# Kernel optimization log

Measured on AMD Instinct MI355X. Metric: run time of the kernel, lower is better.

Reference implementation:

```python
import jax, jax.numpy as jnp
import numpy as np

N_NODES = 100000
N_EDGES = 600000
D = 128  # input_dim == output_dim (required by index_add into zeros_like(x) + residual)
EPS = 1e-5


def _linear_params(key, d_in, d_out):
    kw, kb = jax.random.split(key)
    bound = 1.0 / np.sqrt(d_in)
    w = jax.random.uniform(kw, (d_in, d_out), minval=-bound, maxval=bound, dtype=jnp.float32)
    b = jax.random.uniform(kb, (d_out,), minval=-bound, maxval=bound, dtype=jnp.float32)
    return w, b


def setup_inputs() -> dict:
    key = jax.random.key(0)
    ks = jax.random.split(key, 6)
    x = jax.random.normal(ks[0], (N_NODES, D), dtype=jnp.float32)
    edge_index = jax.random.randint(ks[1], (2, N_EDGES), 0, N_NODES, dtype=jnp.int32)
    w_m1, b_m1 = _linear_params(ks[2], 2 * D, D)
    w_m2, b_m2 = _linear_params(ks[3], D, D)
    w_u1, b_u1 = _linear_params(ks[4], 2 * D, D)
    w_u2, b_u2 = _linear_params(ks[5], D, D)
    gamma = jnp.ones((D,), dtype=jnp.float32)
    beta = jnp.zeros((D,), dtype=jnp.float32)
    return {
        "x": x, "edge_index": edge_index,
        "w_m1": w_m1, "b_m1": b_m1, "w_m2": w_m2, "b_m2": b_m2,
        "w_u1": w_u1, "b_u1": b_u1, "w_u2": w_u2, "b_u2": b_u2,
        "gamma": gamma, "beta": beta,
    }


def _layernorm(h, gamma, beta):
    mu = jnp.mean(h, axis=-1, keepdims=True)
    var = jnp.mean(jnp.square(h - mu), axis=-1, keepdims=True)
    return (h - mu) * jax.lax.rsqrt(var + EPS) * gamma + beta


def reference(x, edge_index, w_m1, b_m1, w_m2, b_m2, w_u1, b_u1, w_u2, b_u2, gamma, beta):
    row, col = edge_index[0], edge_index[1]
    # message MLP on concat of gathered endpoints: [E, 2D] -> [E, D]
    m_in = jnp.concatenate([x[row], x[col]], axis=-1)
    m = jax.nn.relu(m_in @ w_m1 + b_m1) @ w_m2 + b_m2
    # scatter-add messages to destination nodes (index_add along dim 0 with col)
    agg = jax.ops.segment_sum(m, col, num_segments=x.shape[0])
    # update MLP on [N, 2D] -> [N, D]
    u_in = jnp.concatenate([x, agg], axis=-1)
    h = jax.nn.relu(u_in @ w_u1 + b_u1) @ w_u2 + b_u2
    return _layernorm(h, gamma, beta) + x
```

## Files before the change

kernel.cpp:

```cpp
#include <hip/hip_runtime.h>
#include <hip/hip_bf16.h>
#include <stdint.h>

#define N_NODES 100000
#define N_EDGES 600000
#define D 128
#define EPS 1e-5f
#define SCAN_BS 512
#define ROW_MASK 0x1FFFF

#define PREP_BLOCKS 321
#define HIST_BLOCKS 2344
#define XF_BLOCKS   3125
#define SC_BLOCKS   2344
#define AU_BLOCKS   3125

typedef __attribute__((ext_vector_type(8))) short short8;
typedef __attribute__((ext_vector_type(16))) float floatx16;


__device__ __forceinline__ uint32_t pack_bf16_rne(float lo, float hi) {
    uint32_t ul = __builtin_bit_cast(uint32_t, lo);
    uint32_t uh = __builtin_bit_cast(uint32_t, hi);
    ul += 0x7fffu + ((ul >> 16) & 1u);
    uh += 0x7fffu + ((uh >> 16) & 1u);
    return (ul >> 16) | (uh & 0xffff0000u);
}

__device__ __forceinline__ unsigned short f32_to_bf16_rne(float f) {
    uint32_t u = __builtin_bit_cast(uint32_t, f);
    u += 0x7fffu + ((u >> 16) & 1u);
    return (unsigned short)(u >> 16);
}

__device__ __forceinline__ float bflo(uint32_t a) { return __builtin_bit_cast(float, a << 16); }
__device__ __forceinline__ float bfhi(uint32_t a) { return __builtin_bit_cast(float, a & 0xffff0000u); }

__global__ void prep_hist(const float* __restrict__ w_m1, const float* __restrict__ w_u1,
                          const float* __restrict__ w_u2, const float* __restrict__ w_m2,
                          const float* __restrict__ b_m2,
                          unsigned short* __restrict__ wm1f, unsigned short* __restrict__ wu1tf,
                          unsigned short* __restrict__ wu2f, unsigned short* __restrict__ wcf,
                          float* __restrict__ vb,
                          const int* __restrict__ col, int* __restrict__ count,
                          int* __restrict__ rank) {
    if (blockIdx.x >= PREP_BLOCKS) {
        int e = (blockIdx.x - PREP_BLOCKS) * 256 + threadIdx.x;
        if (e < N_EDGES) rank[e] = atomicAdd(&count[col[e]], 1);
        return;
    }
    int idx = blockIdx.x * 256 + threadIdx.x;
    if (idx < 32768) {
        int j = idx & 7, lane = (idx >> 3) & 63, t = (idx >> 9) & 3, s = idx >> 11;
        int kk = s * 16 + ((lane >> 5) << 3) + j;
        wm1f[idx] = f32_to_bf16_rne(w_m1[kk * 128 + t * 32 + (lane & 31)]);
    } else if (idx < 49152) {
        int ii = idx - 32768;
        int j = ii & 7, lane = (ii >> 3) & 63, t = (ii >> 9) & 3, s = ii >> 11;
        int kk = s * 16 + ((lane >> 5) << 3) + j;
        wu1tf[ii] = f32_to_bf16_rne(w_u1[kk * 128 + t * 32 + (lane & 31)]);
    } else if (idx < 65536) {
        int ii = idx - 49152;
        int j = ii & 7, lane = (ii >> 3) & 63, t = (ii >> 9) & 3, s = ii >> 11;
        int kk = s * 16 + ((lane >> 5) << 3) + j;
        wu2f[ii] = f32_to_bf16_rne(w_u2[kk * 128 + t * 32 + (lane & 31)]);
    } else if (idx < 81920) {
        int ii = idx - 65536;
        int j = ii & 7, lane = (ii >> 3) & 63, t = (ii >> 9) & 3, s = ii >> 11;
        int kk = s * 16 + ((lane >> 5) << 3) + j;
        int nn = t * 32 + (lane & 31);
        float acc = 0.0f;
        for (int q = 0; q < 128; ++q)
            acc += w_m2[kk * 128 + q] * w_u1[(128 + q) * 128 + nn];
        wcf[ii] = f32_to_bf16_rne(acc);
    } else if (idx < 82048) {
        int nn = idx - 81920;
        float acc = 0.0f;
        for (int q = 0; q < 128; ++q)
            acc += b_m2[q] * w_u1[(128 + q) * 128 + nn];
        vb[nn] = acc;
    }
}

__global__ void scan_one(const int* __restrict__ count, int* __restrict__ base,
                         int* __restrict__ gcur) {
    __shared__ int tmp[SCAN_BS];
    __shared__ int bbase;
    int g = blockIdx.x * SCAN_BS + threadIdx.x;
    int v = (g < N_NODES) ? count[g] : 0;
    tmp[threadIdx.x] = v;
    __syncthreads();
    int acc = v;
#pragma unroll
    for (int off = 1; off < SCAN_BS; off <<= 1) {
        int add = (threadIdx.x >= off) ? tmp[threadIdx.x - off] : 0;
        __syncthreads();
        acc += add;
        tmp[threadIdx.x] = acc;
        __syncthreads();
    }
    if (threadIdx.x == SCAN_BS - 1) bbase = atomicAdd(gcur, acc);
    __syncthreads();
    if (g < N_NODES) base[g] = bbase + acc - v;
}

__launch_bounds__(64, 4)
__global__ void xform_scatter(const float* __restrict__ x, const short8* __restrict__ w1f,
                              const float* __restrict__ b1, unsigned short* __restrict__ xtb,
                              const int* __restrict__ row, const int* __restrict__ col,
                              const int* __restrict__ rank, const int* __restrict__ base,
                              int* __restrict__ srow) {
    if (blockIdx.x >= XF_BLOCKS) {
        int e4 = (((blockIdx.x - XF_BLOCKS) * 64 + threadIdx.x) << 2);
        if (e4 < N_EDGES) {
            int4 r4 = *(const int4*)(row + e4);
            int4 c4 = *(const int4*)(col + e4);
            int4 k4 = *(const int4*)(rank + e4);
            srow[base[c4.x] + k4.x] = r4.x | ((c4.x & 31) << 17);
            srow[base[c4.y] + k4.y] = r4.y | ((c4.y & 31) << 17);
            srow[base[c4.z] + k4.z] = r4.z | ((c4.z & 31) << 17);
            srow[base[c4.w] + k4.w] = r4.w | ((c4.w & 31) << 17);
        }
        return;
    }

    __shared__ __align__(16) short h1[32 * 136];
    const int lane = threadIdx.x;
    const int l31  = lane & 31;
    const int half = lane >> 5;
    short* hl = h1;

    const int nbase = blockIdx.x * 32;
    const int n = nbase + l31;
    const float* px = x + (size_t)n * D + half * 8;

    union { short8 v; uint32_t u[4]; } fa[8];
#pragma unroll
    for (int s = 0; s < 8; ++s) {
        const int off = s * 16;
        float4 a0 = *(const float4*)(px + off);
        float4 a1 = *(const float4*)(px + off + 4);
        fa[s].u[0] = pack_bf16_rne(a0.x, a0.y); fa[s].u[1] = pack_bf16_rne(a0.z, a0.w);
        fa[s].u[2] = pack_bf16_rne(a1.x, a1.y); fa[s].u[3] = pack_bf16_rne(a1.z, a1.w);
    }

#pragma unroll
    for (int p = 0; p < 2; ++p) {
        floatx16 acc[4];
#pragma unroll
        for (int t = 0; t < 4; ++t) acc[t] = (floatx16)0.0f;
#pragma unroll
        for (int s = 0; s < 8; ++s) {
#pragma unroll
            for (int t = 0; t < 4; ++t) {
                short8 wf = w1f[((p * 8 + s) * 4 + t) * 64 + lane];
                acc[t] = __builtin_amdgcn_mfma_f32_32x32x16_bf16(fa[s].v, wf, acc[t], 0, 0, 0);
            }
        }
#pragma unroll
        for (int t = 0; t < 4; ++t) {
            float bias = p ? b1[t * 32 + l31] : 0.0f;
#pragma unroll
            for (int r = 0; r < 16; ++r) {
                int m = (r & 3) + 8 * (r >> 2) + 4 * half;
                hl[m * 136 + t * 32 + l31] = (short)f32_to_bf16_rne(acc[t][r] + bias);
            }
        }
#pragma unroll
        for (int it = 0; it < 8; ++it) {
            int off = it * 512 + lane * 8;
            int r2 = off >> 7;
            int c2 = off & 127;
            short8 v = *(const short8*)(hl + r2 * 136 + c2);
            *(short8*)(xtb + (size_t)(nbase + r2) * 256 + p * 128 + c2) = v;
        }
    }
}

__launch_bounds__(256, 4)
__global__ void aggupd_kernel(const float* __restrict__ x, const uint32_t* __restrict__ xtb32,
                              const int* __restrict__ srowpk,
                              const int* __restrict__ base, const int* __restrict__ count,
                              const short8* __restrict__ wu1tf, const short8* __restrict__ wcf,
                              const short8* __restrict__ wu2f,
                              const float* __restrict__ b_u1, const float* __restrict__ vb,
                              const float* __restrict__ b_u2,
                              const float* __restrict__ gamma, const float* __restrict__ beta,
                              float* __restrict__ out) {
    __shared__ __align__(16) uint32_t accu[32 * 64];
    __shared__ __align__(16) uint32_t XBl[32 * 64];
    __shared__ __align__(16) short h1[32 * 136];
    __shared__ float partS1[4][32], partS2[4][32];
    __shared__ float meanA[32], rsA[32];

    const int tid  = threadIdx.x;
    const int wv   = tid >> 6;
    const int lane = tid & 63;
    const int l31  = lane & 31;
    const int half = lane >> 5;
    const int t    = lane & 15;
    const int q16  = lane & 48;

    const int nbase = blockIdx.x * 32;

    {
        uint4 z; z.x = 0; z.y = 0; z.z = 0; z.w = 0;
        *((uint4*)accu + tid) = z;
        *((uint4*)accu + 256 + tid) = z;
#pragma unroll
        for (int it = 0; it < 2; ++it) {
            int fi4 = it * 256 + tid;
            int i = fi4 >> 4, k4 = fi4 & 15;
            *((uint4*)XBl + fi4) = *(const uint4*)(xtb32 + (size_t)(nbase + i) * 128 + 64 + (k4 << 2));
        }
    }
    __syncthreads();

    {
        const int nodew = nbase + 8 * wv;
        const int b_l = base[nodew + (lane & 7)];
        const int c_l = count[nodew + (lane & 7)];
        const int qsrc = q16 >> 3;
        const int qbeg = __shfl(b_l, qsrc);
        const int qend = __shfl(b_l, qsrc + 1) + __shfl(c_l, qsrc + 1);
        const int rembase = qend - qbeg;

        int ncm = (rembase + 7) >> 3;
        ncm = max(ncm, __shfl_xor(ncm, 16));
        ncm = max(ncm, __shfl_xor(ncm, 32));

        float sl0 = 0.f, sl1 = 0.f, sl2 = 0.f, sl3 = 0.f;
        float sh0 = 0.f, sh1 = 0.f, sh2 = 0.f, sh3 = 0.f;
        int curnib = -1;

        auto flush = [&]() {
            uint4 o;
            o.x = pack_bf16_rne(sl0, sh0);
            o.y = pack_bf16_rne(sl1, sh1);
            o.z = pack_bf16_rne(sl2, sh2);
            o.w = pack_bf16_rne(sl3, sh3);
            *(uint4*)(accu + (curnib << 6) + (t << 2)) = o;
        };

        for (int c = 0; c < ncm; ++c) {
            int idx = qbeg + (c << 3) + (t & 7);
            int pk = srowpk[min(idx, N_EDGES - 1)];
            const int rem = rembase - (c << 3);

            uint4 xt[8]; int pv[8];
#pragma unroll
            for (int e = 0; e < 8; ++e) {
                int p = __shfl(pk, q16 + e);
                if (e >= rem) p = 0;
                pv[e] = p;
                xt[e] = *(const uint4*)(xtb32 + (size_t)(p & ROW_MASK) * 128 + (t << 2));
            }
            __builtin_amdgcn_sched_barrier(0);
#pragma unroll
            for (int e = 0; e < 8; ++e) {
                if (e < rem) {
                    int nib = pv[e] >> 17;
                    uint4 xb = *(const uint4*)(XBl + (nib << 6) + (t << 2));
                    float a0 = fmaxf(bflo(xt[e].x) + bflo(xb.x), 0.f);
                    float b0 = fmaxf(bfhi(xt[e].x) + bfhi(xb.x), 0.f);
                    float a1 = fmaxf(bflo(xt[e].y) + bflo(xb.y), 0.f);
                    float b1 = fmaxf(bfhi(xt[e].y) + bfhi(xb.y), 0.f);
                    float a2 = fmaxf(bflo(xt[e].z) + bflo(xb.z), 0.f);
                    float b2 = fmaxf(bfhi(xt[e].z) + bfhi(xb.z), 0.f);
                    float a3 = fmaxf(bflo(xt[e].w) + bflo(xb.w), 0.f);
                    float b3 = fmaxf(bfhi(xt[e].w) + bfhi(xb.w), 0.f);
                    if (nib != curnib) {
                        if (curnib >= 0) flush();
                        curnib = nib;
                        sl0 = a0; sh0 = b0; sl1 = a1; sh1 = b1;
                        sl2 = a2; sh2 = b2; sl3 = a3; sh3 = b3;
                    } else {
                        sl0 += a0; sh0 += b0; sl1 += a1; sh1 += b1;
                        sl2 += a2; sh2 += b2; sl3 += a3; sh3 += b3;
                    }
                }
            }
        }
        if (curnib >= 0) flush();
    }
    __syncthreads();

    const int nc = nbase + l31;
    const float dgv = (float)count[nc];
    const float* px = x + (size_t)nc * D + half * 8;

    const float bu1  = b_u1[wv * 32 + l31];
    const float vbt  = vb[wv * 32 + l31];
    const float bias2 = b_u2[wv * 32 + l31];
    const float gA   = gamma[wv * 32 + l31];
    const float beA  = beta[wv * 32 + l31];

    floatx16 acc = (floatx16)0.0f;
#pragma unroll
    for (int s = 0; s < 8; ++s) {
        union { short8 v; uint32_t u[4]; } fa;
        const int off = s * 16;
        float4 a0 = *(const float4*)(px + off);
        float4 a1 = *(const float4*)(px + off + 4);
        fa.u[0] = pack_bf16_rne(a0.x, a0.y); fa.u[1] = pack_bf16_rne(a0.z, a0.w);
        fa.u[2] = pack_bf16_rne(a1.x, a1.y); fa.u[3] = pack_bf16_rne(a1.z, a1.w);
        short8 wf = wu1tf[(s * 4 + wv) * 64 + lane];
        acc = __builtin_amdgcn_mfma_f32_32x32x16_bf16(fa.v, wf, acc, 0, 0, 0);
    }
#pragma unroll
    for (int s = 0; s < 8; ++s) {
        short8 fh = *(const short8*)((const short*)accu + l31 * 128 + s * 16 + half * 8);
        short8 wf = wcf[(s * 4 + wv) * 64 + lane];
        acc = __builtin_amdgcn_mfma_f32_32x32x16_bf16(fh, wf, acc, 0, 0, 0);
    }

#pragma unroll
    for (int r = 0; r < 16; ++r) {
        int m = (r & 3) + 8 * (r >> 2) + 4 * half;
        float dg = __shfl(dgv, m, 32);
        float v = fmaxf(acc[r] + bu1 + dg * vbt, 0.0f);
        h1[m * 136 + wv * 32 + l31] = (short)f32_to_bf16_rne(v);
    }
    __syncthreads();

    short8 af[8];
#pragma unroll
    for (int s = 0; s < 8; ++s)
        af[s] = *(const short8*)(h1 + l31 * 136 + s * 16 + half * 8);
    floatx16 acc2 = (floatx16)0.0f;
#pragma unroll
    for (int s = 0; s < 8; ++s) {
        short8 wf = wu2f[(s * 4 + wv) * 64 + lane];
        acc2 = __builtin_amdgcn_mfma_f32_32x32x16_bf16(af[s], wf, acc2, 0, 0, 0);
    }

#pragma unroll
    for (int r = 0; r < 16; ++r) {
        float hv = acc2[r] + bias2;
        float s1 = hv, s2 = hv * hv;
#pragma unroll
        for (int mask = 1; mask < 32; mask <<= 1) {
            s1 += __shfl_xor(s1, mask);
            s2 += __shfl_xor(s2, mask);
        }
        int m = (r & 3) + 8 * (r >> 2) + 4 * half;
        if (l31 == 0) { partS1[wv][m] = s1; partS2[wv][m] = s2; }
    }
    __syncthreads();
    if (tid < 32) {
        int m = tid;
        float s1 = partS1[0][m] + partS1[1][m] + partS1[2][m] + partS1[3][m];
        float s2 = partS2[0][m] + partS2[1][m] + partS2[2][m] + partS2[3][m];
        float mean = s1 * (1.0f / 128.0f);
        float var  = s2 * (1.0f / 128.0f) - mean * mean;
        meanA[m] = mean;
        rsA[m]   = rsqrtf(var + EPS);
    }
    __syncthreads();

    float* hf = (float*)h1;
#pragma unroll
    for (int p = 0; p < 2; ++p) {
#pragma unroll
        for (int r = 0; r < 16; ++r) {
            int m = (r & 3) + 8 * (r >> 2) + 4 * half;
            int mrow = m - 16 * p;
            if (mrow >= 0 && mrow < 16) {
                float hv = acc2[r] + bias2;
                hf[mrow * 132 + wv * 32 + l31] = (hv - meanA[m]) * rsA[m] * gA + beA;
            }
        }
        __syncthreads();
#pragma unroll
        for (int it = 0; it < 2; ++it) {
            int q = it * 256 + tid;
            int r2 = q >> 5;
            int c4 = q & 31;
            int node = nbase + 16 * p + r2;
            float4 v = *(const float4*)(hf + r2 * 132 + c4 * 4);
            float4 xr = *(const float4*)(x + (size_t)node * D + c4 * 4);
            v.x += xr.x; v.y += xr.y; v.z += xr.z; v.w += xr.w;
            *(float4*)(out + (size_t)node * D + c4 * 4) = v;
        }
        __syncthreads();
    }
}

extern "C" void kernel_launch(void* const* d_in, const int* in_sizes, int n_in,
                              void* d_out, int out_size, void* d_ws, size_t ws_size,
                              hipStream_t stream) {
    const float* x     = (const float*)d_in[0];
    const int*   edge  = (const int*)d_in[1];
    const float* w_m1  = (const float*)d_in[2];
    const float* b_m1  = (const float*)d_in[3];
    const float* w_m2  = (const float*)d_in[4];
    const float* b_m2  = (const float*)d_in[5];
    const float* w_u1  = (const float*)d_in[6];
    const float* b_u1  = (const float*)d_in[7];
    const float* w_u2  = (const float*)d_in[8];
    const float* b_u2  = (const float*)d_in[9];
    const float* gamma = (const float*)d_in[10];
    const float* beta  = (const float*)d_in[11];
    float* out = (float*)d_out;

    char* ws = (char*)d_ws;
    size_t off = 0;
    auto alloc = [&](size_t bytes) { void* p = ws + off; off = (off + bytes + 15) & ~(size_t)15; return p; };

    unsigned short* xtb   = (unsigned short*)alloc((size_t)N_NODES * 256 * 2);
    unsigned short* wm1f  = (unsigned short*)alloc(256 * 128 * 2);
    unsigned short* wu1tf = (unsigned short*)alloc(128 * 128 * 2);
    unsigned short* wcf   = (unsigned short*)alloc(128 * 128 * 2);
    unsigned short* wu2f  = (unsigned short*)alloc(128 * 128 * 2);
    float* vb    = (float*)alloc(128 * 4);
    int* count   = (int*)alloc((size_t)N_NODES * 4 + 16);
    int* gcur    = count + N_NODES;
    int* base    = (int*)alloc((size_t)N_NODES * 4);
    int* rank    = (int*)alloc((size_t)N_EDGES * 4);
    int* srow    = (int*)alloc((size_t)N_EDGES * 4);

    const int* rowi = edge;
    const int* coli = edge + N_EDGES;
    const int NB = (N_NODES + SCAN_BS - 1) / SCAN_BS;

    (void)hipMemsetAsync(count, 0, (size_t)N_NODES * 4 + 16, stream);

    prep_hist<<<PREP_BLOCKS + HIST_BLOCKS, 256, 0, stream>>>(
        w_m1, w_u1, w_u2, w_m2, b_m2, wm1f, wu1tf, wu2f, wcf, vb, coli, count, rank);

    scan_one<<<NB, SCAN_BS, 0, stream>>>(count, base, gcur);

    xform_scatter<<<XF_BLOCKS + SC_BLOCKS, 64, 0, stream>>>(
        x, (const short8*)wm1f, b_m1, xtb, rowi, coli, rank, base, srow);

    aggupd_kernel<<<AU_BLOCKS, 256, 0, stream>>>(
        x, (const uint32_t*)xtb, srow, base, count,
        (const short8*)wu1tf, (const short8*)wcf, (const short8*)wu2f,
        b_u1, vb, b_u2, gamma, beta, out);
}
```

Measured before the change: 261.8 us.

## Split aggregation and update into separate kernels; widen xform blocks to two waves

The fused aggregate+update kernel becomes two kernels. A one-wave aggregation kernel handles 8 nodes per block and writes its bf16 sums back into the second half of the xtb buffer. A separate update kernel then reads those sums from global memory for its MFMAs. xform_scatter now runs two waves per block, one per output half, instead of looping over both halves in one wave. This gives finer-grained blocks for the irregular gather and better load balance, at the cost of an extra launch and a global round-trip for the aggregated features. Overwriting xtb's second half in place is safe only if no other block still reads that region: agg_kernel itself reads the second-half rows of its own 8 nodes into XBl, and if edge rows are ever read from the second half by other blocks, this would be a race.

```diff
diff --git a/kernel.cpp b/kernel.cpp
--- a/kernel.cpp
+++ b/kernel.cpp
@@ -12,8 +12,9 @@
 #define PREP_BLOCKS 321
 #define HIST_BLOCKS 2344
 #define XF_BLOCKS   3125
-#define SC_BLOCKS   2344
-#define AU_BLOCKS   3125
+#define SC_BLOCKS   1172
+#define AGG_BLOCKS  12500
+#define UPD_BLOCKS  3125
 
 typedef __attribute__((ext_vector_type(8))) short short8;
 typedef __attribute__((ext_vector_type(16))) float floatx16;
@@ -104,14 +105,14 @@
     if (g < N_NODES) base[g] = bbase + acc - v;
 }
 
-__launch_bounds__(64, 4)
+__launch_bounds__(128, 4)
 __global__ void xform_scatter(const float* __restrict__ x, const short8* __restrict__ w1f,
                               const float* __restrict__ b1, unsigned short* __restrict__ xtb,
                               const int* __restrict__ row, const int* __restrict__ col,
                               const int* __restrict__ rank, const int* __restrict__ base,
                               int* __restrict__ srow) {
     if (blockIdx.x >= XF_BLOCKS) {
-        int e4 = (((blockIdx.x - XF_BLOCKS) * 64 + threadIdx.x) << 2);
+        int e4 = (((blockIdx.x - XF_BLOCKS) * 128 + threadIdx.x) << 2);
         if (e4 < N_EDGES) {
             int4 r4 = *(const int4*)(row + e4);
             int4 c4 = *(const int4*)(col + e4);
@@ -124,11 +125,13 @@
         return;
     }
 
-    __shared__ __align__(16) short h1[32 * 136];
-    const int lane = threadIdx.x;
+    __shared__ __align__(16) short h1[2][32 * 136];
+    const int wv   = threadIdx.x >> 6;
+    const int lane = threadIdx.x & 63;
     const int l31  = lane & 31;
     const int half = lane >> 5;
-    short* hl = h1;
+    short* hl = h1[wv];
+    const int p = wv;
 
     const int nbase = blockIdx.x * 32;
     const int n = nbase + l31;
@@ -144,91 +147,71 @@
         fa[s].u[2] = pack_bf16_rne(a1.x, a1.y); fa[s].u[3] = pack_bf16_rne(a1.z, a1.w);
     }
 
-#pragma unroll
-    for (int p = 0; p < 2; ++p) {
-        floatx16 acc[4];
-#pragma unroll
-        for (int t = 0; t < 4; ++t) acc[t] = (floatx16)0.0f;
-#pragma unroll
-        for (int s = 0; s < 8; ++s) {
-#pragma unroll
-            for (int t = 0; t < 4; ++t) {
-                short8 wf = w1f[((p * 8 + s) * 4 + t) * 64 + lane];
-                acc[t] = __builtin_amdgcn_mfma_f32_32x32x16_bf16(fa[s].v, wf, acc[t], 0, 0, 0);
-            }
-        }
+    floatx16 acc[4];
+#pragma unroll
+    for (int t = 0; t < 4; ++t) acc[t] = (floatx16)0.0f;
+#pragma unroll
+    for (int s = 0; s < 8; ++s) {
 #pragma unroll
         for (int t = 0; t < 4; ++t) {
-            float bias = p ? b1[t * 32 + l31] : 0.0f;
-#pragma unroll
-            for (int r = 0; r < 16; ++r) {
-                int m = (r & 3) + 8 * (r >> 2) + 4 * half;
-                hl[m * 136 + t * 32 + l31] = (short)f32_to_bf16_rne(acc[t][r] + bias);
-            }
-        }
-#pragma unroll
-        for (int it = 0; it < 8; ++it) {
-            int off = it * 512 + lane * 8;
-            int r2 = off >> 7;
-            int c2 = off & 127;
-            short8 v = *(const short8*)(hl + r2 * 136 + c2);
-            *(short8*)(xtb + (size_t)(nbase + r2) * 256 + p * 128 + c2) = v;
-        }
-    }
-}
-
-__launch_bounds__(256, 4)
-__global__ void aggupd_kernel(const float* __restrict__ x, const uint32_t* __restrict__ xtb32,
-                              const int* __restrict__ srowpk,
-                              const int* __restrict__ base, const int* __restrict__ count,
-                              const short8* __restrict__ wu1tf, const short8* __restrict__ wcf,
-                              const short8* __restrict__ wu2f,
-                              const float* __restrict__ b_u1, const float* __restrict__ vb,
-                              const float* __restrict__ b_u2,
-                              const float* __restrict__ gamma, const float* __restrict__ beta,
-                              float* __restrict__ out) {
-    __shared__ __align__(16) uint32_t accu[32 * 64];
-    __shared__ __align__(16) uint32_t XBl[32 * 64];
-    __shared__ __align__(16) short h1[32 * 136];
-    __shared__ float partS1[4][32], partS2[4][32];
-    __shared__ float meanA[32], rsA[32];
-
-    const int tid  = threadIdx.x;
-    const int wv   = tid >> 6;
-    const int lane = tid & 63;
-    const int l31  = lane & 31;
-    const int half = lane >> 5;
+            short8 wf = w1f[((p * 8 + s) * 4 + t) * 64 + lane];
+            acc[t] = __builtin_amdgcn_mfma_f32_32x32x16_bf16(fa[s].v, wf, acc[t], 0, 0, 0);
+        }
+    }
+#pragma unroll
+    for (int t = 0; t < 4; ++t) {
+        float bias = p ? b1[t * 32 + l31] : 0.0f;
+#pragma unroll
+        for (int r = 0; r < 16; ++r) {
+            int m = (r & 3) + 8 * (r >> 2) + 4 * half;
+            hl[m * 136 + t * 32 + l31] = (short)f32_to_bf16_rne(acc[t][r] + bias);
+        }
+    }
+#pragma unroll
+    for (int it = 0; it < 8; ++it) {
+        int off = it * 512 + lane * 8;
+        int r2 = off >> 7;
+        int c2 = off & 127;
+        short8 v = *(const short8*)(hl + r2 * 136 + c2);
+        *(short8*)(xtb + (size_t)(nbase + r2) * 256 + p * 128 + c2) = v;
+    }
+}
+
+__launch_bounds__(64, 4)
+__global__ void agg_kernel(uint32_t* __restrict__ xtb32, const int* __restrict__ srowpk,
+                           const int* __restrict__ base, const int* __restrict__ count) {
+    __shared__ __align__(16) uint32_t accu[8 * 64];
+    __shared__ __align__(16) uint32_t XBl[8 * 64];
+    const int lane = threadIdx.x;
     const int t    = lane & 15;
     const int q16  = lane & 48;
 
-    const int nbase = blockIdx.x * 32;
+    const int nbase = blockIdx.x * 8;
+
+    const int b_l = base[nbase + (lane & 7)];
+    const int c_l = count[nbase + (lane & 7)];
+    const int qsrc = q16 >> 3;
+    const int qbeg = __shfl(b_l, qsrc);
+    const int qend = __shfl(b_l, qsrc + 1) + __shfl(c_l, qsrc + 1);
+    const int rembase = qend - qbeg;
+
+    int ncm = (rembase + 7) >> 3;
+    ncm = max(ncm, __shfl_xor(ncm, 16));
+    ncm = max(ncm, __shfl_xor(ncm, 32));
 
     {
         uint4 z; z.x = 0; z.y = 0; z.z = 0; z.w = 0;
-        *((uint4*)accu + tid) = z;
-        *((uint4*)accu + 256 + tid) = z;
-#pragma unroll
-        for (int it = 0; it < 2; ++it) {
-            int fi4 = it * 256 + tid;
-            int i = fi4 >> 4, k4 = fi4 & 15;
-            *((uint4*)XBl + fi4) = *(const uint4*)(xtb32 + (size_t)(nbase + i) * 128 + 64 + (k4 << 2));
-        }
-    }
-    __syncthreads();
+        *((uint4*)accu + lane) = z;
+        *((uint4*)accu + 64 + lane) = z;
+    }
+#pragma unroll
+    for (int it = 0; it < 2; ++it) {
+        int fi4 = it * 64 + lane;
+        int i = fi4 >> 4, k4 = fi4 & 15;
+        *((uint4*)XBl + fi4) = *(const uint4*)(xtb32 + (size_t)(nbase + i) * 128 + 64 + (k4 << 2));
+    }
 
     {
-        const int nodew = nbase + 8 * wv;
-        const int b_l = base[nodew + (lane & 7)];
-        const int c_l = count[nodew + (lane & 7)];
-        const int qsrc = q16 >> 3;
-        const int qbeg = __shfl(b_l, qsrc);
-        const int qend = __shfl(b_l, qsrc + 1) + __shfl(c_l, qsrc + 1);
-        const int rembase = qend - qbeg;
-
-        int ncm = (rembase + 7) >> 3;
-        ncm = max(ncm, __shfl_xor(ncm, 16));
-        ncm = max(ncm, __shfl_xor(ncm, 32));
-
         float sl0 = 0.f, sl1 = 0.f, sl2 = 0.f, sl3 = 0.f;
         float sh0 = 0.f, sh1 = 0.f, sh2 = 0.f, sh3 = 0.f;
         int curnib = -1;
@@ -259,7 +242,7 @@
 #pragma unroll
             for (int e = 0; e < 8; ++e) {
                 if (e < rem) {
-                    int nib = pv[e] >> 17;
+                    int nib = (pv[e] >> 17) & 7;
                     uint4 xb = *(const uint4*)(XBl + (nib << 6) + (t << 2));
                     float a0 = fmaxf(bflo(xt[e].x) + bflo(xb.x), 0.f);
                     float b0 = fmaxf(bfhi(xt[e].x) + bfhi(xb.x), 0.f);
@@ -283,17 +266,45 @@
         }
         if (curnib >= 0) flush();
     }
-    __syncthreads();
-
+
+#pragma unroll
+    for (int it = 0; it < 2; ++it) {
+        int fi4 = it * 64 + lane;
+        int i = fi4 >> 4, k4 = fi4 & 15;
+        *(uint4*)(xtb32 + (size_t)(nbase + i) * 128 + 64 + (k4 << 2)) = *((uint4*)accu + fi4);
+    }
+}
+
+__launch_bounds__(256, 4)
+__global__ void upd_kernel(const float* __restrict__ x, const uint32_t* __restrict__ xtb32,
+                           const int* __restrict__ count,
+                           const short8* __restrict__ wu1tf, const short8* __restrict__ wcf,
+                           const short8* __restrict__ wu2f,
+                           const float* __restrict__ b_u1, const float* __restrict__ vb,
+                           const float* __restrict__ b_u2,
+                           const float* __restrict__ gamma, const float* __restrict__ beta,
+                           float* __restrict__ out) {
+    __shared__ __align__(16) short h1[32 * 136];
+    __shared__ float partS1[4][32], partS2[4][32];
+    __shared__ float meanA[32], rsA[32];
+
+    const int tid  = threadIdx.x;
+    const int wv   = tid >> 6;
+    const int lane = tid & 63;
+    const int l31  = lane & 31;
+    const int half = lane >> 5;
+
+    const int nbase = blockIdx.x * 32;
     const int nc = nbase + l31;
     const float dgv = (float)count[nc];
     const float* px = x + (size_t)nc * D + half * 8;
-
-    const float bu1  = b_u1[wv * 32 + l31];
-    const float vbt  = vb[wv * 32 + l31];
+    const short* xtbs = (const short*)xtb32;
+
+    const float bu1   = b_u1[wv * 32 + l31];
+    const float vbt   = vb[wv * 32 + l31];
     const float bias2 = b_u2[wv * 32 + l31];
-    const float gA   = gamma[wv * 32 + l31];
-    const float beA  = beta[wv * 32 + l31];
+    const float gA    = gamma[wv * 32 + l31];
+    const float beA   = beta[wv * 32 + l31];
 
     floatx16 acc = (floatx16)0.0f;
 #pragma unroll
@@ -309,7 +320,7 @@
     }
 #pragma unroll
     for (int s = 0; s < 8; ++s) {
-        short8 fh = *(const short8*)((const short*)accu + l31 * 128 + s * 16 + half * 8);
+        short8 fh = *(const short8*)(xtbs + (size_t)nc * 256 + 128 + s * 16 + half * 8);
         short8 wf = wcf[(s * 4 + wv) * 64 + lane];
         acc = __builtin_amdgcn_mfma_f32_32x32x16_bf16(fh, wf, acc, 0, 0, 0);
     }
@@ -430,11 +441,14 @@
 
     scan_one<<<NB, SCAN_BS, 0, stream>>>(count, base, gcur);
 
-    xform_scatter<<<XF_BLOCKS + SC_BLOCKS, 64, 0, stream>>>(
+    xform_scatter<<<XF_BLOCKS + SC_BLOCKS, 128, 0, stream>>>(
         x, (const short8*)wm1f, b_m1, xtb, rowi, coli, rank, base, srow);
 
-    aggupd_kernel<<<AU_BLOCKS, 256, 0, stream>>>(
-        x, (const uint32_t*)xtb, srow, base, count,
+    agg_kernel<<<AGG_BLOCKS, 64, 0, stream>>>(
+        (uint32_t*)xtb, srow, base, count);
+
+    upd_kernel<<<UPD_BLOCKS, 256, 0, stream>>>(
+        x, (const uint32_t*)xtb, count,
         (const short8*)wu1tf, (const short8*)wcf, (const short8*)wu2f,
         b_u1, vb, b_u2, gamma, beta, out);
 }
```

New measurement: 275.7 us. 1.05x slower.
